# Kernel optimization log

Hardware: AMD Instinct MI355X
Metric: run time of the kernel (lower is better)

The kernel has to match this reference:

```python
import jax, jax.numpy as jnp
import numpy as np

N = 50000
E = 800000
G = 16  # graphs in batch
NEG_SLOPE = 0.2


def gatv2_layer(x, src, dst, Wl, bl, Wr, br, att, bias, concat):
    # PyG GATv2Conv: x_j = lin_l(x)[src], x_i = lin_r(x)[dst]
    H, C = att.shape
    n = x.shape[0]
    xl = (x @ Wl + bl).reshape(n, H, C)  # source transform
    xr = (x @ Wr + br).reshape(n, H, C)  # target transform
    e = jax.nn.leaky_relu(xl[src] + xr[dst], NEG_SLOPE)  # [E,H,C]
    score = jnp.einsum('ehc,hc->eh', e, att)             # [E,H]
    # segment softmax over incoming edges of each dst node
    smax = jax.ops.segment_max(score, dst, num_segments=n)   # [n,H]
    ex = jnp.exp(score - smax[dst])
    denom = jax.ops.segment_sum(ex, dst, num_segments=n)
    alpha = ex / (denom[dst] + 1e-16)                        # [E,H]
    out = jax.ops.segment_sum(alpha[:, :, None] * xl[src], dst, num_segments=n)  # [n,H,C]
    if concat:
        return out.reshape(n, H * C) + bias
    return out.mean(axis=1) + bias


def setup_inputs() -> dict:
    key = jax.random.key(0)
    ks = jax.random.split(key, 20)
    x = jax.random.normal(ks[0], (N, 8), dtype=jnp.float32)
    edge_index = jax.random.randint(ks[1], (2, E), 0, N, dtype=jnp.int64)
    batch = jnp.sort(jax.random.randint(ks[2], (N,), 0, G, dtype=jnp.int64))

    def glorot(k, shape):
        lim = np.sqrt(6.0 / (shape[0] + shape[1]))
        return jax.random.uniform(k, shape, jnp.float32, -lim, lim)

    params = dict(
        Wl1=glorot(ks[3], (8, 128)), bl1=jnp.zeros((128,), jnp.float32),
        Wr1=glorot(ks[4], (8, 128)), br1=jnp.zeros((128,), jnp.float32),
        att1=glorot(ks[5], (2, 64)), b1=jnp.zeros((128,), jnp.float32),
        Wl2=glorot(ks[6], (128, 128)), bl2=jnp.zeros((128,), jnp.float32),
        Wr2=glorot(ks[7], (128, 128)), br2=jnp.zeros((128,), jnp.float32),
        att2=glorot(ks[8], (2, 64)), b2=jnp.zeros((128,), jnp.float32),
        Wl3=glorot(ks[9], (128, 32)), bl3=jnp.zeros((32,), jnp.float32),
        Wr3=glorot(ks[10], (128, 32)), br3=jnp.zeros((32,), jnp.float32),
        att3=glorot(ks[11], (1, 32)), b3=jnp.zeros((32,), jnp.float32),
    )
    return dict(x=x, edge_index=edge_index, batch=batch, **params)


def reference(x, edge_index, batch,
              Wl1, bl1, Wr1, br1, att1, b1,
              Wl2, bl2, Wr2, br2, att2, b2,
              Wl3, bl3, Wr3, br3, att3, b3):
    n = x.shape[0]
    loops = jnp.arange(n, dtype=edge_index.dtype)
    src = jnp.concatenate([edge_index[0], loops])  # add_self_loops=True (PyG default)
    dst = jnp.concatenate([edge_index[1], loops])

    h = gatv2_layer(x, src, dst, Wl1, bl1, Wr1, br1, att1, b1, concat=True)
    h = jax.nn.elu(h)
    # dropout(p=0.5) is identity in eval mode
    h = gatv2_layer(h, src, dst, Wl2, bl2, Wr2, br2, att2, b2, concat=True)
    h = jax.nn.elu(h)
    h = gatv2_layer(h, src, dst, Wl3, bl3, Wr3, br3, att3, b3, concat=False)
    h = jax.nn.elu(h)  # [n,32]

    counts = jax.ops.segment_sum(jnp.ones((n,), h.dtype), batch, num_segments=G)
    pooled_mean = jax.ops.segment_sum(h, batch, num_segments=G) / counts[:, None]
    pooled_max = jax.ops.segment_max(h, batch, num_segments=G)
    return jnp.concatenate([pooled_mean, pooled_max], axis=1)  # [G,64]
```

## Files before the change

kernel.cpp:

```cpp
#include <hip/hip_runtime.h>
#include <hip/hip_bf16.h>
#include <math.h>


__device__ __forceinline__ float lrelu(float x) { return x > 0.f ? x : 0.2f * x; }
__device__ __forceinline__ float elu1(float x) { return x > 0.f ? x : expm1f(x); }

__device__ __forceinline__ unsigned f2ord(float x) {
    unsigned b = __float_as_uint(x);
    return (b & 0x80000000u) ? ~b : (b | 0x80000000u);
}
__device__ __forceinline__ float ord2f(unsigned u) {
    unsigned b = (u & 0x80000000u) ? (u & 0x7FFFFFFFu) : ~u;
    return __uint_as_float(b);
}
__device__ __forceinline__ unsigned short f2bf(float f) {
    unsigned u = __float_as_uint(f);
    unsigned r = u + 0x7FFFu + ((u >> 16) & 1u);
    return (unsigned short)(r >> 16);
}

__global__ void k_zero_i32(int* __restrict__ p, int n) {
    int i = blockIdx.x * blockDim.x + threadIdx.x;
    if (i < n) p[i] = 0;
}

__global__ void k_hist(const int* __restrict__ ei, int E, int N, int* __restrict__ deg) {
    int e = blockIdx.x * blockDim.x + threadIdx.x;
    int Etot = E + N;
    if (e >= Etot) return;
    int d = (e < E) ? ei[E + e] : (e - E);
    atomicAdd(&deg[d], 1);
}

__global__ void __launch_bounds__(1024) k_scan_blk(
        const int* __restrict__ deg, int n,
        int* __restrict__ part, int* __restrict__ bsum) {
    __shared__ int wsum[16];
    int tid = threadIdx.x;
    int lane = tid & 63, w = tid >> 6;
    int i = blockIdx.x * 1024 + tid;
    int v = (i < n) ? deg[i] : 0;
    int s = v;
    #pragma unroll
    for (int d = 1; d < 64; d <<= 1) {
        int t = __shfl_up(s, d, 64);
        if (lane >= d) s += t;
    }
    if (lane == 63) wsum[w] = s;
    __syncthreads();
    int wbase = 0;
    for (int k = 0; k < w; k++) wbase += wsum[k];
    if (i < n) part[i] = wbase + (s - v);
    if (tid == 1023) bsum[blockIdx.x] = wbase + s;
}

__global__ void k_scan_top(const int* __restrict__ bsum, int nb,
                           int* __restrict__ boff, int* __restrict__ row_off, int n) {
    int lane = threadIdx.x;
    int base = 0;
    for (int st = 0; st < nb; st += 64) {
        int i = st + lane;
        int v = (i < nb) ? bsum[i] : 0;
        int s = v;
        #pragma unroll
        for (int d = 1; d < 64; d <<= 1) {
            int t = __shfl_up(s, d, 64);
            if (lane >= d) s += t;
        }
        if (i < nb) boff[i] = base + (s - v);
        base += __shfl(s, 63, 64);
    }
    if (lane == 0) row_off[n] = base;
}

__global__ void __launch_bounds__(1024) k_scan_add(
        const int* __restrict__ part, const int* __restrict__ boff, int n,
        int* __restrict__ row_off, int* __restrict__ cursor) {
    int i = blockIdx.x * 1024 + threadIdx.x;
    if (i < n) {
        int r = part[i] + boff[blockIdx.x];
        row_off[i] = r;
        cursor[i] = r;
    }
}

__global__ void k_scatter(const int* __restrict__ ei, int E, int N,
                          int* __restrict__ cursor,
                          int* __restrict__ csr_src) {
    int e = blockIdx.x * blockDim.x + threadIdx.x;
    int Etot = E + N;
    if (e >= Etot) return;
    int s, d;
    if (e < E) { s = ei[e]; d = ei[E + e]; } else { s = e - E; d = e - E; }
    int p = atomicAdd(&cursor[d], 1);
    csr_src[p] = s;
}

template <int K>
__global__ void k_linear2b(const float* __restrict__ x, int N,
                           const float* __restrict__ Wl, const float* __restrict__ bl,
                           const float* __restrict__ Wr, const float* __restrict__ br,
                           unsigned short* __restrict__ xlb, float* __restrict__ xr) {
    constexpr int MH = 128, NCG = 64;
    __shared__ float xs[32 * K];
    int tid = threadIdx.x;
    int node0 = blockIdx.x * 32;
    for (int idx = tid * 4; idx < 32 * K; idx += NCG * 4 * 4) {
        int node = node0 + idx / K;
        float4 v = make_float4(0.f, 0.f, 0.f, 0.f);
        if (node < N) v = *(const float4*)(x + (size_t)node0 * K + idx);
        *(float4*)(xs + idx) = v;
    }
    __syncthreads();

    int cg = tid % NCG;
    int ng = tid / NCG;
    bool rightSide = cg >= (MH / 4);
    int c = (rightSide ? cg - MH / 4 : cg) * 4;
    const float* W  = rightSide ? Wr : Wl;
    const float* bb = rightSide ? br : bl;

    float acc[8][4];
    #pragma unroll
    for (int i = 0; i < 8; i++)
        #pragma unroll
        for (int j = 0; j < 4; j++) acc[i][j] = 0.f;

    const float* xrow = xs + ng * 8 * K;
    for (int k0 = 0; k0 < K; k0 += 4) {
        float4 wv[4];
        #pragma unroll
        for (int kk = 0; kk < 4; kk++)
            wv[kk] = *(const float4*)(W + (size_t)(k0 + kk) * MH + c);
        #pragma unroll
        for (int i = 0; i < 8; i++) {
            float4 xv = *(const float4*)(xrow + i * K + k0);
            float xvk[4] = {xv.x, xv.y, xv.z, xv.w};
            #pragma unroll
            for (int kk = 0; kk < 4; kk++) {
                acc[i][0] += xvk[kk] * wv[kk].x;
                acc[i][1] += xvk[kk] * wv[kk].y;
                acc[i][2] += xvk[kk] * wv[kk].z;
                acc[i][3] += xvk[kk] * wv[kk].w;
            }
        }
    }
    float4 bv = *(const float4*)(bb + c);
    #pragma unroll
    for (int i = 0; i < 8; i++) {
        int node = node0 + ng * 8 + i;
        if (node >= N) continue;
        float o0 = acc[i][0] + bv.x, o1 = acc[i][1] + bv.y;
        float o2 = acc[i][2] + bv.z, o3 = acc[i][3] + bv.w;
        if (rightSide) {
            *(float4*)(xr + (size_t)node * MH + c) = make_float4(o0, o1, o2, o3);
        } else {
            ushort4 ub = make_ushort4(f2bf(o0), f2bf(o1), f2bf(o2), f2bf(o3));
            *(ushort4*)(xlb + (size_t)node * MH + c) = ub;
        }
    }
}

__global__ void __launch_bounds__(256) k_linear3(
        const float* __restrict__ x, int N,
        const float* __restrict__ Wl, const float* __restrict__ bl,
        const float* __restrict__ Wr, const float* __restrict__ br,
        float* __restrict__ xl, float* __restrict__ xr) {
    __shared__ float xs[32 * 128];
    int tid = threadIdx.x;
    int node0 = blockIdx.x * 32;
    for (int idx = tid * 4; idx < 32 * 128; idx += 256 * 4) {
        int node = node0 + idx / 128;
        float4 v = make_float4(0.f, 0.f, 0.f, 0.f);
        if (node < N) v = *(const float4*)(x + (size_t)node0 * 128 + idx);
        *(float4*)(xs + idx) = v;
    }
    __syncthreads();
    int cg = tid & 15, ng = tid >> 4;
    bool rightSide = cg >= 8;
    int c = (rightSide ? cg - 8 : cg) * 4;
    const float* W  = rightSide ? Wr : Wl;
    const float* bb = rightSide ? br : bl;
    float* out      = rightSide ? xr : xl;

    float acc[2][4];
    #pragma unroll
    for (int i = 0; i < 2; i++)
        #pragma unroll
        for (int j = 0; j < 4; j++) acc[i][j] = 0.f;

    const float* xrow = xs + ng * 2 * 128;
    for (int k0 = 0; k0 < 128; k0 += 4) {
        float4 wv[4];
        #pragma unroll
        for (int kk = 0; kk < 4; kk++)
            wv[kk] = *(const float4*)(W + (size_t)(k0 + kk) * 32 + c);
        #pragma unroll
        for (int i = 0; i < 2; i++) {
            float4 xv = *(const float4*)(xrow + i * 128 + k0);
            float xvk[4] = {xv.x, xv.y, xv.z, xv.w};
            #pragma unroll
            for (int kk = 0; kk < 4; kk++) {
                acc[i][0] += xvk[kk] * wv[kk].x;
                acc[i][1] += xvk[kk] * wv[kk].y;
                acc[i][2] += xvk[kk] * wv[kk].z;
                acc[i][3] += xvk[kk] * wv[kk].w;
            }
        }
    }
    float4 bv = *(const float4*)(bb + c);
    #pragma unroll
    for (int i = 0; i < 2; i++) {
        int node = node0 + ng * 2 + i;
        if (node < N) {
            float4 o = make_float4(acc[i][0] + bv.x, acc[i][1] + bv.y,
                                   acc[i][2] + bv.z, acc[i][3] + bv.w);
            *(float4*)(out + (size_t)node * 32 + c) = o;
        }
    }
}

__device__ __forceinline__ void unpack8(int4 rv, float* v) {
    unsigned u0 = (unsigned)rv.x, u1 = (unsigned)rv.y;
    unsigned u2 = (unsigned)rv.z, u3 = (unsigned)rv.w;
    v[0] = __uint_as_float(u0 << 16); v[1] = __uint_as_float(u0 & 0xFFFF0000u);
    v[2] = __uint_as_float(u1 << 16); v[3] = __uint_as_float(u1 & 0xFFFF0000u);
    v[4] = __uint_as_float(u2 << 16); v[5] = __uint_as_float(u2 & 0xFFFF0000u);
    v[6] = __uint_as_float(u3 << 16); v[7] = __uint_as_float(u3 & 0xFFFF0000u);
}

__global__ void k_fusedb(const int* __restrict__ row_off, const int* __restrict__ csr_src,
                         const unsigned short* __restrict__ xlb, const float* __restrict__ xr,
                         const float* __restrict__ att, const float* __restrict__ bias,
                         float* __restrict__ hout, int N) {
    constexpr int HC = 128, CPL = 8, GROUP = 8;
    int wid = (blockIdx.x * blockDim.x + threadIdx.x) >> 6;
    int lane = threadIdx.x & 63;
    if (wid >= N) return;
    int slot = lane >> 4;
    int j = lane & 15;
    int c0 = j * CPL;

    int p0 = row_off[wid], p1 = row_off[wid + 1];

    float xrv[CPL], attv[CPL];
    {
        float4 a = *(const float4*)(xr + (size_t)wid * HC + c0);
        float4 b = *(const float4*)(xr + (size_t)wid * HC + c0 + 4);
        xrv[0] = a.x; xrv[1] = a.y; xrv[2] = a.z; xrv[3] = a.w;
        xrv[4] = b.x; xrv[5] = b.y; xrv[6] = b.z; xrv[7] = b.w;
        float4 c = *(const float4*)(att + c0);
        float4 d = *(const float4*)(att + c0 + 4);
        attv[0] = c.x; attv[1] = c.y; attv[2] = c.z; attv[3] = c.w;
        attv[4] = d.x; attv[5] = d.y; attv[6] = d.z; attv[7] = d.w;
    }

    float m = -INFINITY, den = 0.f;
    float acc[CPL];
    #pragma unroll
    for (int q = 0; q < CPL; q++) acc[q] = 0.f;

    int p = p0 + slot;
    int s0 = (p < p1) ? csr_src[p] : 0;
    int s1 = (p + 4 < p1) ? csr_src[p + 4] : 0;
    while (p < p1) {
        int np = p + 8;
        int ns0 = (np < p1) ? csr_src[np] : 0;
        int ns1 = (np + 4 < p1) ? csr_src[np + 4] : 0;
        bool has2 = (p + 4) < p1;
        int4 ra = *(const int4*)(xlb + (size_t)s0 * HC + c0);
        int4 rb = *(const int4*)(xlb + (size_t)s1 * HC + c0);
        float xa[CPL], xb[CPL];
        unpack8(ra, xa);
        unpack8(rb, xb);
        float pa = 0.f, pb = 0.f;
        #pragma unroll
        for (int q = 0; q < CPL; q++) {
            float ta = xa[q] + xrv[q];
            float tb = xb[q] + xrv[q];
            pa = fmaf(fmaxf(ta, 0.2f * ta), attv[q], pa);
            pb = fmaf(fmaxf(tb, 0.2f * tb), attv[q], pb);
        }
        #pragma unroll
        for (int msk = 1; msk < GROUP; msk <<= 1) {
            pa += __shfl_xor(pa, msk, 64);
            pb += __shfl_xor(pb, msk, 64);
        }
        if (pa > m + 8.f) {
            float corr = __expf(m - pa);
            den *= corr;
            #pragma unroll
            for (int q = 0; q < CPL; q++) acc[q] *= corr;
            m = pa;
        }
        float ea = __expf(pa - m);
        den += ea;
        #pragma unroll
        for (int q = 0; q < CPL; q++) acc[q] = fmaf(ea, xa[q], acc[q]);
        if (has2) {
            if (pb > m + 8.f) {
                float corr = __expf(m - pb);
                den *= corr;
                #pragma unroll
                for (int q = 0; q < CPL; q++) acc[q] *= corr;
                m = pb;
            }
            float eb = __expf(pb - m);
            den += eb;
            #pragma unroll
            for (int q = 0; q < CPL; q++) acc[q] = fmaf(eb, xb[q], acc[q]);
        }
        p = np; s0 = ns0; s1 = ns1;
    }
    float mAll = fmaxf(m, __shfl_xor(m, 16, 64));
    mAll = fmaxf(mAll, __shfl_xor(mAll, 32, 64));
    float scale = __expf(m - mAll);
    float dtot = den * scale;
    dtot += __shfl_xor(dtot, 16, 64);
    dtot += __shfl_xor(dtot, 32, 64);
    #pragma unroll
    for (int q = 0; q < CPL; q++) {
        float a = acc[q] * scale;
        a += __shfl_xor(a, 16, 64);
        a += __shfl_xor(a, 32, 64);
        acc[q] = a;
    }
    if (slot == 0) {
        float inv = 1.0f / (dtot + 1e-16f);
        #pragma unroll
        for (int q = 0; q < CPL; q++) {
            float v = acc[q] * inv + bias[c0 + q];
            hout[(size_t)wid * HC + c0 + q] = elu1(v);
        }
    }
}

template <int CPL>
__device__ __forceinline__ void loadrow(const float* __restrict__ p, float* v) {
    if constexpr (CPL == 8) {
        float4 a = ((const float4*)p)[0];
        float4 b = ((const float4*)p)[1];
        v[0] = a.x; v[1] = a.y; v[2] = a.z; v[3] = a.w;
        v[4] = b.x; v[5] = b.y; v[6] = b.z; v[7] = b.w;
    } else {
        float2 a = ((const float2*)p)[0];
        v[0] = a.x; v[1] = a.y;
    }
}

template <int HC, int C>
__global__ void k_fused(const int* __restrict__ row_off, const int* __restrict__ csr_src,
                        const float* __restrict__ xl, const float* __restrict__ xr,
                        const float* __restrict__ att, const float* __restrict__ bias,
                        float* __restrict__ hout, int N) {
    constexpr int CPL = HC / 16;
    constexpr int GROUP = (16 * C) / HC;
    int wid = (blockIdx.x * blockDim.x + threadIdx.x) >> 6;
    int lane = threadIdx.x & 63;
    if (wid >= N) return;
    int slot = lane >> 4;
    int j = lane & 15;
    int c0 = j * CPL;

    int p0 = row_off[wid], p1 = row_off[wid + 1];

    float xrv[CPL], attv[CPL];
    loadrow<CPL>(xr + (size_t)wid * HC + c0, xrv);
    loadrow<CPL>(att + c0, attv);

    float m = -INFINITY, den = 0.f;
    float acc[CPL];
    #pragma unroll
    for (int q = 0; q < CPL; q++) acc[q] = 0.f;

    int p = p0 + slot;
    int s = (p < p1) ? csr_src[p] : 0;
    while (p < p1) {
        int pn = p + 4;
        int sn = (pn < p1) ? csr_src[pn] : 0;
        float xlv[CPL];
        loadrow<CPL>(xl + (size_t)s * HC + c0, xlv);
        float part = 0.f;
        #pragma unroll
        for (int q = 0; q < CPL; q++) {
            float t = xlv[q] + xrv[q];
            part = fmaf(fmaxf(t, 0.2f * t), attv[q], part);
        }
        #pragma unroll
        for (int msk = 1; msk < GROUP; msk <<= 1) part += __shfl_xor(part, msk, 64);
        if (part > m + 8.f) {
            float corr = __expf(m - part);
            den *= corr;
            #pragma unroll
            for (int q = 0; q < CPL; q++) acc[q] *= corr;
            m = part;
        }
        float ex = __expf(part - m);
        den += ex;
        #pragma unroll
        for (int q = 0; q < CPL; q++) acc[q] = fmaf(ex, xlv[q], acc[q]);
        p = pn; s = sn;
    }
    float mAll = fmaxf(m, __shfl_xor(m, 16, 64));
    mAll = fmaxf(mAll, __shfl_xor(mAll, 32, 64));
    float scale = __expf(m - mAll);
    float dtot = den * scale;
    dtot += __shfl_xor(dtot, 16, 64);
    dtot += __shfl_xor(dtot, 32, 64);
    #pragma unroll
    for (int q = 0; q < CPL; q++) {
        float a = acc[q] * scale;
        a += __shfl_xor(a, 16, 64);
        a += __shfl_xor(a, 32, 64);
        acc[q] = a;
    }
    if (slot == 0) {
        float inv = 1.0f / (dtot + 1e-16f);
        #pragma unroll
        for (int q = 0; q < CPL; q++) {
            float v = acc[q] * inv + bias[c0 + q];
            hout[(size_t)wid * HC + c0 + q] = elu1(v);
        }
    }
}

__global__ void __launch_bounds__(256) k_pool_partial(
        const float* __restrict__ h, const int* __restrict__ batch, int N, int G,
        float* __restrict__ gsum, unsigned* __restrict__ gmax) {
    __shared__ float lsum[512];
    __shared__ unsigned lmax[512];
    int tid = threadIdx.x;
    for (int i = tid; i < G * 32; i += 256) { lsum[i] = 0.f; lmax[i] = 0u; }
    __syncthreads();
    int chunk = (N + gridDim.x - 1) / gridDim.x;
    int start = blockIdx.x * chunk;
    int end = min(N, start + chunk);
    int col = tid & 31, row = tid >> 5;
    int gc = -1; float ps = 0.f; unsigned pm = 0u;
    for (int i = start + row; i < end; i += 8) {
        int g = batch[i];
        if (g != gc) {
            if (gc >= 0) { atomicAdd(&lsum[gc * 32 + col], ps); atomicMax(&lmax[gc * 32 + col], pm); }
            gc = g; ps = 0.f; pm = 0u;
        }
        float v = h[(size_t)i * 32 + col];
        ps += v; pm = max(pm, f2ord(v));
    }
    if (gc >= 0) { atomicAdd(&lsum[gc * 32 + col], ps); atomicMax(&lmax[gc * 32 + col], pm); }
    __syncthreads();
    for (int i = tid; i < G * 32; i += 256) {
        if (lmax[i]) {
            atomicAdd(&gsum[i], lsum[i]);
            atomicMax(&gmax[i], lmax[i]);
        }
    }
}

__global__ void k_pool_final(const float* __restrict__ gsum, const unsigned* __restrict__ gmax,
                             const int* __restrict__ batch, int N, float* __restrict__ out) {
    int g = blockIdx.x;
    int t = threadIdx.x;
    __shared__ int s_cnt;
    if (t == 0) {
        int lo = 0, hi = N;
        while (lo < hi) { int m = (lo + hi) >> 1; if (batch[m] < g) lo = m + 1; else hi = m; }
        int a = lo;
        lo = a; hi = N;
        while (lo < hi) { int m = (lo + hi) >> 1; if (batch[m] < g + 1) lo = m + 1; else hi = m; }
        s_cnt = lo - a;
    }
    __syncthreads();
    if (t < 32) {
        out[g * 64 + t] = gsum[g * 32 + t] / (float)max(s_cnt, 1);
    } else {
        out[g * 64 + t] = ord2f(gmax[g * 32 + (t - 32)]);
    }
}

extern "C" void kernel_launch(void* const* d_in, const int* in_sizes, int n_in,
                              void* d_out, int out_size, void* d_ws, size_t ws_size,
                              hipStream_t stream) {
    const float* x      = (const float*)d_in[0];
    const int*   ei     = (const int*)d_in[1];
    const int*   batch  = (const int*)d_in[2];
    const float* Wl1 = (const float*)d_in[3],  *bl1 = (const float*)d_in[4];
    const float* Wr1 = (const float*)d_in[5],  *br1 = (const float*)d_in[6];
    const float* att1= (const float*)d_in[7],  *b1  = (const float*)d_in[8];
    const float* Wl2 = (const float*)d_in[9],  *bl2 = (const float*)d_in[10];
    const float* Wr2 = (const float*)d_in[11], *br2 = (const float*)d_in[12];
    const float* att2= (const float*)d_in[13], *b2  = (const float*)d_in[14];
    const float* Wl3 = (const float*)d_in[15], *bl3 = (const float*)d_in[16];
    const float* Wr3 = (const float*)d_in[17], *br3 = (const float*)d_in[18];
    const float* att3= (const float*)d_in[19], *b3  = (const float*)d_in[20];

    int N = in_sizes[0] / 8;
    int E = in_sizes[1] / 2;
    int G = out_size / 64;
    int Etot = E + N;
    int nb = (N + 1023) / 1024;

    char* w = (char*)d_ws;
    auto carve = [&](size_t bytes) {
        void* p = (void*)w;
        w += (bytes + 255) & ~(size_t)255;
        return p;
    };
    int*            deg     = (int*)carve((size_t)N * 4);
    int*            row_off = (int*)carve((size_t)(N + 1) * 4);
    int*            cursor  = (int*)carve((size_t)N * 4);
    int*            part    = (int*)carve((size_t)N * 4);
    int*            bsum    = (int*)carve((size_t)nb * 4);
    int*            boff    = (int*)carve((size_t)nb * 4);
    int*            csr_src = (int*)carve((size_t)Etot * 4);
    float*          gsum    = (float*)carve((size_t)G * 32 * 4);
    unsigned*       gmax    = (unsigned*)carve((size_t)G * 32 * 4);
    unsigned short* xlb     = (unsigned short*)carve((size_t)N * 128 * 2);
    float*          bufA    = (float*)carve((size_t)N * 128 * 4);
    float*          bufB    = (float*)carve((size_t)N * 128 * 4);
    float*          bufC    = (float*)carve((size_t)N * 128 * 4);
    (void)ws_size; (void)n_in;

    k_zero_i32<<<(N + 255) / 256, 256, 0, stream>>>(deg, N);
    k_zero_i32<<<(2 * G * 32 + 255) / 256, 256, 0, stream>>>((int*)gsum, 2 * G * 32);
    k_hist<<<(Etot + 255) / 256, 256, 0, stream>>>(ei, E, N, deg);
    k_scan_blk<<<nb, 1024, 0, stream>>>(deg, N, part, bsum);
    k_scan_top<<<1, 64, 0, stream>>>(bsum, nb, boff, row_off, N);
    k_scan_add<<<nb, 1024, 0, stream>>>(part, boff, N, row_off, cursor);
    k_scatter<<<(Etot + 255) / 256, 256, 0, stream>>>(ei, E, N, cursor, csr_src);

    int grdLin = (N + 31) / 32;
    int grdFused = (N + 3) / 4;

    k_linear2b<8><<<grdLin, 256, 0, stream>>>(x, N, Wl1, bl1, Wr1, br1, xlb, bufB);
    k_fusedb<<<grdFused, 256, 0, stream>>>(row_off, csr_src, xlb, bufB, att1, b1, bufC, N);

    k_linear2b<128><<<grdLin, 256, 0, stream>>>(bufC, N, Wl2, bl2, Wr2, br2, xlb, bufB);
    k_fusedb<<<grdFused, 256, 0, stream>>>(row_off, csr_src, xlb, bufB, att2, b2, bufC, N);

    k_linear3<<<grdLin, 256, 0, stream>>>(bufC, N, Wl3, bl3, Wr3, br3, bufA, bufB);
    k_fused<32, 32><<<grdFused, 256, 0, stream>>>(row_off, csr_src, bufA, bufB, att3, b3, bufC, N);

    k_pool_partial<<<256, 256, 0, stream>>>(bufC, batch, N, G, gsum, gmax);
    k_pool_final<<<G, 64, 0, stream>>>(gsum, gmax, batch, N, (float*)d_out);
}
```

Before: 481.3 us.

## Split GAT attention aggregation per head into separate wavefronts with 8 edge slots

The 128-wide layers now launch two wavefronts per node, one per attention head. Each uses 8 lanes per edge and 8 edge slots instead of 16 lanes and 4 slots with a two-edge unroll, which doubles the waves in flight for the gather-bound loop. The 32-wide last layer gets a dedicated kernel with 8 lanes per edge over float4 rows instead of 16 lanes over float2, also with 8 edge slots. The cost is an extra cross-slot reduction step, a duplicated read of row offsets and edge indices per head, and each wave now fetches only 16 bytes per lane per edge.

After: 518.9 us. +7.8%, slower.

```diff
diff --git a/kernel.cpp b/kernel.cpp
--- a/kernel.cpp
+++ b/kernel.cpp
@@ -230,24 +230,26 @@
     v[6] = __uint_as_float(u3 << 16); v[7] = __uint_as_float(u3 & 0xFFFF0000u);
 }
 
-__global__ void k_fusedb(const int* __restrict__ row_off, const int* __restrict__ csr_src,
-                         const unsigned short* __restrict__ xlb, const float* __restrict__ xr,
-                         const float* __restrict__ att, const float* __restrict__ bias,
-                         float* __restrict__ hout, int N) {
-    constexpr int HC = 128, CPL = 8, GROUP = 8;
-    int wid = (blockIdx.x * blockDim.x + threadIdx.x) >> 6;
+__global__ void __launch_bounds__(256) k_fusedb(
+        const int* __restrict__ row_off, const int* __restrict__ csr_src,
+        const unsigned short* __restrict__ xlb, const float* __restrict__ xr,
+        const float* __restrict__ att, const float* __restrict__ bias,
+        float* __restrict__ hout, int N) {
+    constexpr int HC = 128, CPL = 8;
+    int gw = (blockIdx.x * blockDim.x + threadIdx.x) >> 6;
+    int node = gw >> 1, head = gw & 1;
     int lane = threadIdx.x & 63;
-    if (wid >= N) return;
-    int slot = lane >> 4;
-    int j = lane & 15;
-    int c0 = j * CPL;
-
-    int p0 = row_off[wid], p1 = row_off[wid + 1];
+    if (node >= N) return;
+    int slot = lane >> 3;
+    int j = lane & 7;
+    int c0 = head * 64 + j * CPL;
+
+    int p0 = row_off[node], p1 = row_off[node + 1];
 
     float xrv[CPL], attv[CPL];
     {
-        float4 a = *(const float4*)(xr + (size_t)wid * HC + c0);
-        float4 b = *(const float4*)(xr + (size_t)wid * HC + c0 + 4);
+        float4 a = *(const float4*)(xr + (size_t)node * HC + c0);
+        float4 b = *(const float4*)(xr + (size_t)node * HC + c0 + 4);
         xrv[0] = a.x; xrv[1] = a.y; xrv[2] = a.z; xrv[3] = a.w;
         xrv[4] = b.x; xrv[5] = b.y; xrv[6] = b.z; xrv[7] = b.w;
         float4 c = *(const float4*)(att + c0);
@@ -262,133 +264,22 @@
     for (int q = 0; q < CPL; q++) acc[q] = 0.f;
 
     int p = p0 + slot;
-    int s0 = (p < p1) ? csr_src[p] : 0;
-    int s1 = (p + 4 < p1) ? csr_src[p + 4] : 0;
-    while (p < p1) {
-        int np = p + 8;
-        int ns0 = (np < p1) ? csr_src[np] : 0;
-        int ns1 = (np + 4 < p1) ? csr_src[np + 4] : 0;
-        bool has2 = (p + 4) < p1;
-        int4 ra = *(const int4*)(xlb + (size_t)s0 * HC + c0);
-        int4 rb = *(const int4*)(xlb + (size_t)s1 * HC + c0);
-        float xa[CPL], xb[CPL];
-        unpack8(ra, xa);
-        unpack8(rb, xb);
-        float pa = 0.f, pb = 0.f;
-        #pragma unroll
-        for (int q = 0; q < CPL; q++) {
-            float ta = xa[q] + xrv[q];
-            float tb = xb[q] + xrv[q];
-            pa = fmaf(fmaxf(ta, 0.2f * ta), attv[q], pa);
-            pb = fmaf(fmaxf(tb, 0.2f * tb), attv[q], pb);
-        }
-        #pragma unroll
-        for (int msk = 1; msk < GROUP; msk <<= 1) {
-            pa += __shfl_xor(pa, msk, 64);
-            pb += __shfl_xor(pb, msk, 64);
-        }
-        if (pa > m + 8.f) {
-            float corr = __expf(m - pa);
-            den *= corr;
-            #pragma unroll
-            for (int q = 0; q < CPL; q++) acc[q] *= corr;
-            m = pa;
-        }
-        float ea = __expf(pa - m);
-        den += ea;
-        #pragma unroll
-        for (int q = 0; q < CPL; q++) acc[q] = fmaf(ea, xa[q], acc[q]);
-        if (has2) {
-            if (pb > m + 8.f) {
-                float corr = __expf(m - pb);
-                den *= corr;
-                #pragma unroll
-                for (int q = 0; q < CPL; q++) acc[q] *= corr;
-                m = pb;
-            }
-            float eb = __expf(pb - m);
-            den += eb;
-            #pragma unroll
-            for (int q = 0; q < CPL; q++) acc[q] = fmaf(eb, xb[q], acc[q]);
-        }
-        p = np; s0 = ns0; s1 = ns1;
-    }
-    float mAll = fmaxf(m, __shfl_xor(m, 16, 64));
-    mAll = fmaxf(mAll, __shfl_xor(mAll, 32, 64));
-    float scale = __expf(m - mAll);
-    float dtot = den * scale;
-    dtot += __shfl_xor(dtot, 16, 64);
-    dtot += __shfl_xor(dtot, 32, 64);
-    #pragma unroll
-    for (int q = 0; q < CPL; q++) {
-        float a = acc[q] * scale;
-        a += __shfl_xor(a, 16, 64);
-        a += __shfl_xor(a, 32, 64);
-        acc[q] = a;
-    }
-    if (slot == 0) {
-        float inv = 1.0f / (dtot + 1e-16f);
-        #pragma unroll
-        for (int q = 0; q < CPL; q++) {
-            float v = acc[q] * inv + bias[c0 + q];
-            hout[(size_t)wid * HC + c0 + q] = elu1(v);
-        }
-    }
-}
-
-template <int CPL>
-__device__ __forceinline__ void loadrow(const float* __restrict__ p, float* v) {
-    if constexpr (CPL == 8) {
-        float4 a = ((const float4*)p)[0];
-        float4 b = ((const float4*)p)[1];
-        v[0] = a.x; v[1] = a.y; v[2] = a.z; v[3] = a.w;
-        v[4] = b.x; v[5] = b.y; v[6] = b.z; v[7] = b.w;
-    } else {
-        float2 a = ((const float2*)p)[0];
-        v[0] = a.x; v[1] = a.y;
-    }
-}
-
-template <int HC, int C>
-__global__ void k_fused(const int* __restrict__ row_off, const int* __restrict__ csr_src,
-                        const float* __restrict__ xl, const float* __restrict__ xr,
-                        const float* __restrict__ att, const float* __restrict__ bias,
-                        float* __restrict__ hout, int N) {
-    constexpr int CPL = HC / 16;
-    constexpr int GROUP = (16 * C) / HC;
-    int wid = (blockIdx.x * blockDim.x + threadIdx.x) >> 6;
-    int lane = threadIdx.x & 63;
-    if (wid >= N) return;
-    int slot = lane >> 4;
-    int j = lane & 15;
-    int c0 = j * CPL;
-
-    int p0 = row_off[wid], p1 = row_off[wid + 1];
-
-    float xrv[CPL], attv[CPL];
-    loadrow<CPL>(xr + (size_t)wid * HC + c0, xrv);
-    loadrow<CPL>(att + c0, attv);
-
-    float m = -INFINITY, den = 0.f;
-    float acc[CPL];
-    #pragma unroll
-    for (int q = 0; q < CPL; q++) acc[q] = 0.f;
-
-    int p = p0 + slot;
     int s = (p < p1) ? csr_src[p] : 0;
     while (p < p1) {
-        int pn = p + 4;
+        int pn = p + 8;
         int sn = (pn < p1) ? csr_src[pn] : 0;
+        int4 rv = *(const int4*)(xlb + (size_t)s * HC + c0);
         float xlv[CPL];
-        loadrow<CPL>(xl + (size_t)s * HC + c0, xlv);
+        unpack8(rv, xlv);
         float part = 0.f;
         #pragma unroll
         for (int q = 0; q < CPL; q++) {
             float t = xlv[q] + xrv[q];
             part = fmaf(fmaxf(t, 0.2f * t), attv[q], part);
         }
-        #pragma unroll
-        for (int msk = 1; msk < GROUP; msk <<= 1) part += __shfl_xor(part, msk, 64);
+        part += __shfl_xor(part, 1, 64);
+        part += __shfl_xor(part, 2, 64);
+        part += __shfl_xor(part, 4, 64);
         if (part > m + 8.f) {
             float corr = __expf(m - part);
             den *= corr;
@@ -402,15 +293,18 @@
         for (int q = 0; q < CPL; q++) acc[q] = fmaf(ex, xlv[q], acc[q]);
         p = pn; s = sn;
     }
-    float mAll = fmaxf(m, __shfl_xor(m, 16, 64));
+    float mAll = fmaxf(m, __shfl_xor(m, 8, 64));
+    mAll = fmaxf(mAll, __shfl_xor(mAll, 16, 64));
     mAll = fmaxf(mAll, __shfl_xor(mAll, 32, 64));
     float scale = __expf(m - mAll);
     float dtot = den * scale;
+    dtot += __shfl_xor(dtot, 8, 64);
     dtot += __shfl_xor(dtot, 16, 64);
     dtot += __shfl_xor(dtot, 32, 64);
     #pragma unroll
     for (int q = 0; q < CPL; q++) {
         float a = acc[q] * scale;
+        a += __shfl_xor(a, 8, 64);
         a += __shfl_xor(a, 16, 64);
         a += __shfl_xor(a, 32, 64);
         acc[q] = a;
@@ -420,7 +314,87 @@
         #pragma unroll
         for (int q = 0; q < CPL; q++) {
             float v = acc[q] * inv + bias[c0 + q];
-            hout[(size_t)wid * HC + c0 + q] = elu1(v);
+            hout[(size_t)node * HC + c0 + q] = elu1(v);
+        }
+    }
+}
+
+__global__ void __launch_bounds__(256) k_fused3(
+        const int* __restrict__ row_off, const int* __restrict__ csr_src,
+        const float* __restrict__ xl, const float* __restrict__ xr,
+        const float* __restrict__ att, const float* __restrict__ bias,
+        float* __restrict__ hout, int N) {
+    constexpr int HC = 32, CPL = 4;
+    int node = (blockIdx.x * blockDim.x + threadIdx.x) >> 6;
+    int lane = threadIdx.x & 63;
+    if (node >= N) return;
+    int slot = lane >> 3;
+    int j = lane & 7;
+    int c0 = j * CPL;
+
+    int p0 = row_off[node], p1 = row_off[node + 1];
+
+    float4 xrq = *(const float4*)(xr + (size_t)node * HC + c0);
+    float4 atq = *(const float4*)(att + c0);
+    float xrv[CPL] = {xrq.x, xrq.y, xrq.z, xrq.w};
+    float attv[CPL] = {atq.x, atq.y, atq.z, atq.w};
+
+    float m = -INFINITY, den = 0.f;
+    float acc[CPL];
+    #pragma unroll
+    for (int q = 0; q < CPL; q++) acc[q] = 0.f;
+
+    int p = p0 + slot;
+    int s = (p < p1) ? csr_src[p] : 0;
+    while (p < p1) {
+        int pn = p + 8;
+        int sn = (pn < p1) ? csr_src[pn] : 0;
+        float4 xq = *(const float4*)(xl + (size_t)s * HC + c0);
+        float xlv[CPL] = {xq.x, xq.y, xq.z, xq.w};
+        float part = 0.f;
+        #pragma unroll
+        for (int q = 0; q < CPL; q++) {
+            float t = xlv[q] + xrv[q];
+            part = fmaf(fmaxf(t, 0.2f * t), attv[q], part);
+        }
+        part += __shfl_xor(part, 1, 64);
+        part += __shfl_xor(part, 2, 64);
+        part += __shfl_xor(part, 4, 64);
+        if (part > m + 8.f) {
+            float corr = __expf(m - part);
+            den *= corr;
+            #pragma unroll
+            for (int q = 0; q < CPL; q++) acc[q] *= corr;
+            m = part;
+        }
+        float ex = __expf(part - m);
+        den += ex;
+        #pragma unroll
+        for (int q = 0; q < CPL; q++) acc[q] = fmaf(ex, xlv[q], acc[q]);
+        p = pn; s = sn;
+    }
+    float mAll = fmaxf(m, __shfl_xor(m, 8, 64));
+    mAll = fmaxf(mAll, __shfl_xor(mAll, 16, 64));
+    mAll = fmaxf(mAll, __shfl_xor(mAll, 32, 64));
+    float scale = __expf(m - mAll);
+    float dtot = den * scale;
+    dtot += __shfl_xor(dtot, 8, 64);
+    dtot += __shfl_xor(dtot, 16, 64);
+    dtot += __shfl_xor(dtot, 32, 64);
+    #pragma unroll
+    for (int q = 0; q < CPL; q++) {
+        float a = acc[q] * scale;
+        a += __shfl_xor(a, 8, 64);
+        a += __shfl_xor(a, 16, 64);
+        a += __shfl_xor(a, 32, 64);
+        acc[q] = a;
+    }
+    if (slot == 0) {
+        float inv = 1.0f / (dtot + 1e-16f);
+        #pragma unroll
+        for (int q = 0; q < CPL; q++) {
+            float v = acc[q] * inv + bias[c0 + q];
+            hout[(size_t)node * HC + c0 + q] = elu1(v);
         }
     }
 }
@@ -530,16 +504,17 @@
     k_scatter<<<(Etot + 255) / 256, 256, 0, stream>>>(ei, E, N, cursor, csr_src);
 
     int grdLin = (N + 31) / 32;
-    int grdFused = (N + 3) / 4;
+    int grdFused  = (N + 3) / 4;
+    int grdFusedH = (2 * N + 3) / 4;
 
     k_linear2b<8><<<grdLin, 256, 0, stream>>>(x, N, Wl1, bl1, Wr1, br1, xlb, bufB);
-    k_fusedb<<<grdFused, 256, 0, stream>>>(row_off, csr_src, xlb, bufB, att1, b1, bufC, N);
+    k_fusedb<<<grdFusedH, 256, 0, stream>>>(row_off, csr_src, xlb, bufB, att1, b1, bufC, N);
 
     k_linear2b<128><<<grdLin, 256, 0, stream>>>(bufC, N, Wl2, bl2, Wr2, br2, xlb, bufB);
-    k_fusedb<<<grdFused, 256, 0, stream>>>(row_off, csr_src, xlb, bufB, att2, b2, bufC, N);
+    k_fusedb<<<grdFusedH, 256, 0, stream>>>(row_off, csr_src, xlb, bufB, att2, b2, bufC, N);
 
     k_linear3<<<grdLin, 256, 0, stream>>>(bufC, N, Wl3, bl3, Wr3, br3, bufA, bufB);
-    k_fused<32, 32><<<grdFused, 256, 0, stream>>>(row_off, csr_src, bufA, bufB, att3, b3, bufC, N);
+    k_fused3<<<grdFused, 256, 0, stream>>>(row_off, csr_src, bufA, bufB, att3, b3, bufC, N);
 
     k_pool_partial<<<256, 256, 0, stream>>>(bufC, batch, N, G, gsum, gmax);
     k_pool_final<<<G, 64, 0, stream>>>(gsum, gmax, batch, N, (float*)d_out);
```
